# Optimization experiments

Measured on AMD Instinct MI355X. Metric: run time of the kernel, lower is better.

Reference implementation:

```python
import jax, jax.numpy as jnp
import numpy as np

DIM = 1024
HEADS = 16
DIM_HEAD = DIM // HEADS

def setup_inputs() -> dict:
    key = jax.random.key(0)
    k1, k2, k3 = jax.random.split(key, 3)
    x = jax.random.normal(k1, (2, 2048, DIM), dtype=jnp.float32)
    # nn.Linear(dim, 3*dim, bias=False): weight [3*dim, dim]; y = x @ W.T
    W_qkv = jax.random.normal(k2, (3 * DIM, DIM), dtype=jnp.float32) * (1.0 / np.sqrt(DIM))
    W_out = jax.random.normal(k3, (DIM, DIM), dtype=jnp.float32) * (1.0 / np.sqrt(DIM))
    return {"x": x, "W_qkv": W_qkv, "W_out": W_out}

def reference(x, W_qkv, W_out):
    b, s, _ = x.shape
    scale = DIM_HEAD ** -0.5
    qkv = x @ W_qkv.T                              # [b, s, 3*dim]
    q, k, v = jnp.split(qkv, 3, axis=-1)
    def to_heads(t):
        return t.reshape(b, s, HEADS, DIM_HEAD).transpose(0, 2, 1, 3)  # [b,h,s,d]
    q, k, v = map(to_heads, (q, k, v))
    scores = jnp.einsum('bhid,bhjd->bhij', q, k) * scale
    causal_mask = jnp.triu(jnp.ones((s, s), dtype=bool), k=1)
    scores = jnp.where(causal_mask, -jnp.inf, scores)
    attn = jax.nn.softmax(scores, axis=-1)
    out = jnp.einsum('bhij,bhjd->bhid', attn, v)
    out = out.transpose(0, 2, 1, 3).reshape(b, s, HEADS * DIM_HEAD)
    return out @ W_out.T
```

## Files before the change

kernel.cpp:

```cpp
#include <hip/hip_runtime.h>
#include <hip/hip_bf16.h>
#include <math.h>

using bf16 = __hip_bfloat16;
typedef __attribute__((ext_vector_type(8))) short bf16x8;
typedef __attribute__((ext_vector_type(4))) short bf16x4;
typedef __attribute__((ext_vector_type(4))) float f32x4;
typedef __attribute__((ext_vector_type(2))) int i32x2;

static __device__ __forceinline__ void gl_lds16(const void* g, void* l) {
  __builtin_amdgcn_global_load_lds(
      (const __attribute__((address_space(1))) unsigned int*)g,
      (__attribute__((address_space(3))) unsigned int*)l, 16, 0, 0);
}

#define MFMA16 __builtin_amdgcn_mfma_f32_16x16x32_bf16
#define MFMA16K16 __builtin_amdgcn_mfma_f32_16x16x16bf16_1k

static __device__ __forceinline__ short f2bf(float f) {
  return (short)((__builtin_bit_cast(unsigned int, f) + 0x8000u) >> 16);
}

__global__ __launch_bounds__(256) void cvt_all(
    const float* __restrict__ x, const float* __restrict__ wqkv,
    const float* __restrict__ wout, bf16* __restrict__ xb,
    bf16* __restrict__ wqkvb, bf16* __restrict__ woutb) {
  const int blk = blockIdx.x;
  const float* src;
  bf16* dst;
  int base;
  if (blk < 4096) {
    src = x; dst = xb; base = blk;
  } else if (blk < 7168) {
    src = wqkv; dst = wqkvb; base = blk - 4096;
  } else {
    src = wout; dst = woutb; base = blk - 7168;
  }
  const int i = (base * 256 + threadIdx.x) * 4;
  const float4 v = *(const float4*)(src + i);
  bf16x4 o;
  o.x = f2bf(v.x);
  o.y = f2bf(v.y);
  o.z = f2bf(v.z);
  o.w = f2bf(v.w);
  *(bf16x4*)(dst + i) = o;
}

template <int K>
static __device__ __forceinline__ void gemm_bt_acc(
    const bf16* __restrict__ A, const bf16* __restrict__ B,
    int rowA0, int rowB0, bf16* As, bf16* Bs, f32x4 acc[4][4]) {
  const int t = threadIdx.x;
  const int w = t >> 6, l = t & 63;
  const int quad = l >> 4, l16 = l & 15;
  const int wm = (w >> 1) * 64, wn = (w & 1) * 64;
  const int c0 = t, c1 = t + 256;
  const bf16* a0 = A + (size_t)(rowA0 + (c0 >> 2)) * K + (c0 & 3) * 8;
  const bf16* a1 = A + (size_t)(rowA0 + (c1 >> 2)) * K + (c1 & 3) * 8;
  const bf16* b0 = B + (size_t)(rowB0 + (c0 >> 2)) * K + (c0 & 3) * 8;
  const bf16* b1 = B + (size_t)(rowB0 + (c1 >> 2)) * K + (c1 & 3) * 8;
  for (int k0 = 0; k0 < K; k0 += 32) {
    __syncthreads();
    gl_lds16(a0 + k0, As + c0 * 8);
    gl_lds16(a1 + k0, As + c1 * 8);
    gl_lds16(b0 + k0, Bs + c0 * 8);
    gl_lds16(b1 + k0, Bs + c1 * 8);
    __syncthreads();
    bf16x8 af[4], bg[4];
#pragma unroll
    for (int i = 0; i < 4; i++)
      af[i] = *(const bf16x8*)(As + (wm + i * 16 + l16) * 32 + quad * 8);
#pragma unroll
    for (int j = 0; j < 4; j++)
      bg[j] = *(const bf16x8*)(Bs + (wn + j * 16 + l16) * 32 + quad * 8);
#pragma unroll
    for (int i = 0; i < 4; i++)
#pragma unroll
      for (int j = 0; j < 4; j++)
        acc[i][j] = MFMA16(af[i], bg[j], acc[i][j], 0, 0, 0);
  }
}

__global__ __launch_bounds__(256) void qkv_gemm(
    const bf16* __restrict__ x, const bf16* __restrict__ Wqkv,
    bf16* __restrict__ Qb, bf16* __restrict__ Kb, bf16* __restrict__ Vt) {
  __shared__ bf16 As[128 * 32];
  __shared__ bf16 Bs[128 * 32];
  f32x4 acc[4][4];
#pragma unroll
  for (int i = 0; i < 4; i++)
#pragma unroll
    for (int j = 0; j < 4; j++) acc[i][j] = (f32x4){0.f, 0.f, 0.f, 0.f};
  const int bm = blockIdx.x, bn = blockIdx.y;
  gemm_bt_acc<1024>(x, Wqkv, bm * 128, bn * 128, As, Bs, acc);

  const int t = threadIdx.x, w = t >> 6, l = t & 63;
  const int quad = l >> 4, l16 = l & 15;
  const int wm = (w >> 1) * 64, wn = (w & 1) * 64;
#pragma unroll
  for (int i = 0; i < 4; i++) {
    const int m0 = bm * 128 + wm + i * 16 + quad * 4;
    const int b = m0 >> 11, s0 = m0 & 2047;
#pragma unroll
    for (int j = 0; j < 4; j++) {
      const int n = bn * 128 + wn + j * 16 + l16;
      const int which = n >> 10;
      const int nn = n & 1023;
      const int h = nn >> 6, d = nn & 63;
      const int bh = b * 16 + h;
      if (which == 2) {
        bf16x4 v4;
#pragma unroll
        for (int r = 0; r < 4; r++)
          v4[r] = (short)__builtin_bit_cast(unsigned short,
                                            __float2bfloat16(acc[i][j][r]));
        *(bf16x4*)(Vt + ((size_t)bh * 64 + d) * 2048 + s0) = v4;
      } else {
        const float sc = (which == 0) ? 0.125f : 1.0f;
        bf16* dst = (which == 0) ? Qb : Kb;
#pragma unroll
        for (int r = 0; r < 4; r++)
          dst[((size_t)bh * 2048 + s0 + r) * 64 + d] =
              __float2bfloat16(acc[i][j][r] * sc);
      }
    }
  }
}

__global__ __launch_bounds__(256, 4) void attn_kernel(
    const bf16* __restrict__ Qb, const bf16* __restrict__ Kb,
    const bf16* __restrict__ Vt, bf16* __restrict__ attn) {
  __shared__ bf16 Ks[128 * 64];
  __shared__ bf16 Vts[64 * 128];
  const int x = blockIdx.x;
  const int bh = x & 31;
  const int T = x >> 5;
  const int s = T >> 3, r = T & 7;
  const int qt = s * 8 + ((s & 1) ? 7 - r : r);
  const int q0 = qt * 64;
  const int t = threadIdx.x, w = t >> 6, l = t & 63;
  const int quad = l >> 4, l16 = l & 15;
  const bf16x4 ones = {16256, 16256, 16256, 16256};
  const int b = bh >> 4, h = bh & 15;

  const int qrow = q0 + w * 16 + l16;
  const bf16* Qg = Qb + ((size_t)bh * 2048 + qrow) * 64 + quad * 8;
  bf16x8 qreg[2];
  qreg[0] = *(const bf16x8*)(Qg);
  qreg[1] = *(const bf16x8*)(Qg + 32);

  f32x4 oacc[4];
  f32x4 lacc = (f32x4){0.f, 0.f, 0.f, 0.f};
#pragma unroll
  for (int md = 0; md < 4; md++) oacc[md] = (f32x4){0.f, 0.f, 0.f, 0.f};

  const int njj = (qt + 2) >> 1;
  for (int jj = 0; jj < njj; jj++) {
    const int j0 = jj * 128;
    __syncthreads();
    const bf16* Kg = Kb + ((size_t)bh * 2048 + j0) * 64;
#pragma unroll
    for (int c = t; c < 1024; c += 256) {
      const int row = c >> 3, pos = c & 7;
      gl_lds16(Kg + (row * 8 + (pos ^ (row & 7))) * 8, Ks + c * 8);
    }
    const bf16* Vg = Vt + (size_t)bh * 64 * 2048 + j0;
#pragma unroll
    for (int c = t; c < 1024; c += 256) {
      const int d = c >> 4, pos = c & 15;
      gl_lds16(Vg + (size_t)d * 2048 + ((pos ^ (d & 15)) * 8), Vts + c * 8);
    }
    __syncthreads();

    f32x4 sacc[8];
#pragma unroll
    for (int mt = 0; mt < 8; mt++) sacc[mt] = (f32x4){0.f, 0.f, 0.f, 0.f};
#pragma unroll
    for (int kk = 0; kk < 2; kk++) {
#pragma unroll
      for (int mt = 0; mt < 8; mt++) {
        const int row = mt * 16 + l16;
        const int pos = (kk * 4 + quad) ^ (row & 7);
        bf16x8 kf = *(const bf16x8*)(Ks + row * 64 + pos * 8);
        sacc[mt] = MFMA16(kf, qreg[kk], sacc[mt], 0, 0, 0);
      }
    }

    bf16x4 pfrag[8];
    if (jj == njj - 1) {
      const int qi = q0 + w * 16 + l16;
#pragma unroll
      for (int mt = 0; mt < 8; mt++) {
        unsigned rb[4];
#pragma unroll
        for (int r2 = 0; r2 < 4; r2++) {
          const int sg = j0 + mt * 16 + quad * 4 + r2;
          const float p = (sg <= qi) ? __expf(sacc[mt][r2]) : 0.f;
          rb[r2] = __builtin_bit_cast(unsigned, p) + 0x8000u;
        }
        i32x2 pk;
        pk.x = (int)__builtin_amdgcn_perm(rb[1], rb[0], 0x07060302u);
        pk.y = (int)__builtin_amdgcn_perm(rb[3], rb[2], 0x07060302u);
        pfrag[mt] = __builtin_bit_cast(bf16x4, pk);
      }
    } else {
#pragma unroll
      for (int mt = 0; mt < 8; mt++) {
        unsigned rb[4];
#pragma unroll
        for (int r2 = 0; r2 < 4; r2++) {
          const float p = __expf(sacc[mt][r2]);
          rb[r2] = __builtin_bit_cast(unsigned, p) + 0x8000u;
        }
        i32x2 pk;
        pk.x = (int)__builtin_amdgcn_perm(rb[1], rb[0], 0x07060302u);
        pk.y = (int)__builtin_amdgcn_perm(rb[3], rb[2], 0x07060302u);
        pfrag[mt] = __builtin_bit_cast(bf16x4, pk);
      }
    }

#pragma unroll
    for (int kt = 0; kt < 8; kt++) {
      lacc = MFMA16K16(ones, pfrag[kt], lacc, 0, 0, 0);
#pragma unroll
      for (int md = 0; md < 4; md++) {
        const int d = md * 16 + l16;
        const int pos = (kt * 2 + (quad >> 1)) ^ (d & 15);
        bf16x4 va = *(const bf16x4*)(Vts + d * 128 + pos * 8 + (quad & 1) * 4);
        oacc[md] = MFMA16K16(va, pfrag[kt], oacc[md], 0, 0, 0);
      }
    }
  }

  const float inv = 1.0f / lacc[0];
#pragma unroll
  for (int md = 0; md < 4; md++) {
    bf16x4 o4;
#pragma unroll
    for (int r2 = 0; r2 < 4; r2++) o4[r2] = f2bf(oacc[md][r2] * inv);
    *(bf16x4*)(attn + ((size_t)b * 2048 + qrow) * 1024 + h * 64 + md * 16 +
               quad * 4) = o4;
  }
}

__global__ __launch_bounds__(256) void out_gemm(
    const bf16* __restrict__ attn, const bf16* __restrict__ Wout,
    float* __restrict__ out) {
  __shared__ bf16 As[128 * 32];
  __shared__ bf16 Bs[64 * 32];
  f32x4 acc[4][2];
#pragma unroll
  for (int i = 0; i < 4; i++)
#pragma unroll
    for (int j = 0; j < 2; j++) acc[i][j] = (f32x4){0.f, 0.f, 0.f, 0.f};
  const int bm = blockIdx.x, bn = blockIdx.y;
  const int t = threadIdx.x, w = t >> 6, l = t & 63;
  const int quad = l >> 4, l16 = l & 15;
  const int wm = (w >> 1) * 64, wn = (w & 1) * 32;
  const int c0 = t, c1 = t + 256;
  const bf16* a0 = attn + (size_t)(bm * 128 + (c0 >> 2)) * 1024 + (c0 & 3) * 8;
  const bf16* a1 = attn + (size_t)(bm * 128 + (c1 >> 2)) * 1024 + (c1 & 3) * 8;
  const bf16* b0 = Wout + (size_t)(bn * 64 + (t >> 2)) * 1024 + (t & 3) * 8;
  for (int k0 = 0; k0 < 1024; k0 += 32) {
    __syncthreads();
    gl_lds16(a0 + k0, As + c0 * 8);
    gl_lds16(a1 + k0, As + c1 * 8);
    gl_lds16(b0 + k0, Bs + t * 8);
    __syncthreads();
    bf16x8 af[4], bg[2];
#pragma unroll
    for (int i = 0; i < 4; i++)
      af[i] = *(const bf16x8*)(As + (wm + i * 16 + l16) * 32 + quad * 8);
#pragma unroll
    for (int j = 0; j < 2; j++)
      bg[j] = *(const bf16x8*)(Bs + (wn + j * 16 + l16) * 32 + quad * 8);
#pragma unroll
    for (int i = 0; i < 4; i++)
#pragma unroll
      for (int j = 0; j < 2; j++)
        acc[i][j] = MFMA16(af[i], bg[j], acc[i][j], 0, 0, 0);
  }
#pragma unroll
  for (int i = 0; i < 4; i++) {
#pragma unroll
    for (int j = 0; j < 2; j++) {
      const int n = bn * 64 + wn + j * 16 + l16;
#pragma unroll
      for (int r = 0; r < 4; r++) {
        const int m = bm * 128 + wm + i * 16 + quad * 4 + r;
        out[(size_t)m * 1024 + n] = acc[i][j][r];
      }
    }
  }
}

extern "C" void kernel_launch(void* const* d_in, const int* in_sizes, int n_in,
                              void* d_out, int out_size, void* d_ws, size_t ws_size,
                              hipStream_t stream) {
  const float* x = (const float*)d_in[0];
  const float* Wqkv = (const float*)d_in[1];
  const float* Wout = (const float*)d_in[2];
  float* out = (float*)d_out;

  char* ws = (char*)d_ws;
  const size_t MB = 1024 * 1024;
  bf16* xb = (bf16*)(ws + 0 * MB);
  bf16* at = (bf16*)(ws + 0 * MB);
  bf16* Wqkvb = (bf16*)(ws + 8 * MB);
  bf16* Woutb = (bf16*)(ws + 14 * MB);
  bf16* Qb = (bf16*)(ws + 16 * MB);
  bf16* Kb = (bf16*)(ws + 24 * MB);
  bf16* Vt = (bf16*)(ws + 32 * MB);

  cvt_all<<<8192, 256, 0, stream>>>(x, Wqkv, Wout, xb, Wqkvb, Woutb);
  qkv_gemm<<<dim3(32, 24), 256, 0, stream>>>(xb, Wqkvb, Qb, Kb, Vt);
  attn_kernel<<<1024, 256, 0, stream>>>(Qb, Kb, Vt, at);
  out_gemm<<<dim3(32, 16), 256, 0, stream>>>(at, Woutb, out);
}
```

Baseline: 164.1 us.

## Halve attention query tile and split key tiles across wave pairs

Each attention block now covers 32 query rows instead of 64, which doubles the grid to 2048 blocks. Within a block, two wave pairs each handle half of every 128-key tile. The partial output and row-sum accumulators are then combined through shared memory before normalisation, and launch bounds are raised to allow five blocks per CU. The aim is better load balance and occupancy for the causal workload, at the cost of loading each K/V tile for fewer queries and an extra LDS reduction at the end.

```diff
diff --git a/kernel.cpp b/kernel.cpp
--- a/kernel.cpp
+++ b/kernel.cpp
@@ -127,7 +127,7 @@
   }
 }
 
-__global__ __launch_bounds__(256, 4) void attn_kernel(
+__global__ __launch_bounds__(256, 5) void attn_kernel(
     const bf16* __restrict__ Qb, const bf16* __restrict__ Kb,
     const bf16* __restrict__ Vt, bf16* __restrict__ attn) {
   __shared__ bf16 Ks[128 * 64];
@@ -137,13 +137,15 @@
   const int T = x >> 5;
   const int s = T >> 3, r = T & 7;
   const int qt = s * 8 + ((s & 1) ? 7 - r : r);
-  const int q0 = qt * 64;
+  const int q0 = qt * 32;
   const int t = threadIdx.x, w = t >> 6, l = t & 63;
   const int quad = l >> 4, l16 = l & 15;
+  const int qh = w & 1;
+  const int kh = w >> 1;
   const bf16x4 ones = {16256, 16256, 16256, 16256};
   const int b = bh >> 4, h = bh & 15;
 
-  const int qrow = q0 + w * 16 + l16;
+  const int qrow = q0 + qh * 16 + l16;
   const bf16* Qg = Qb + ((size_t)bh * 2048 + qrow) * 64 + quad * 8;
   bf16x8 qreg[2];
   qreg[0] = *(const bf16x8*)(Qg);
@@ -154,7 +156,7 @@
 #pragma unroll
   for (int md = 0; md < 4; md++) oacc[md] = (f32x4){0.f, 0.f, 0.f, 0.f};
 
-  const int njj = (qt + 2) >> 1;
+  const int njj = (qt + 4) >> 2;
   for (int jj = 0; jj < njj; jj++) {
     const int j0 = jj * 128;
     __syncthreads();
@@ -172,74 +174,92 @@
     }
     __syncthreads();
 
-    f32x4 sacc[8];
-#pragma unroll
-    for (int mt = 0; mt < 8; mt++) sacc[mt] = (f32x4){0.f, 0.f, 0.f, 0.f};
+    f32x4 sacc[4];
+#pragma unroll
+    for (int m = 0; m < 4; m++) sacc[m] = (f32x4){0.f, 0.f, 0.f, 0.f};
 #pragma unroll
     for (int kk = 0; kk < 2; kk++) {
 #pragma unroll
-      for (int mt = 0; mt < 8; mt++) {
-        const int row = mt * 16 + l16;
-        const int pos = (kk * 4 + quad) ^ (row & 7);
+      for (int m = 0; m < 4; m++) {
+        const int row = (kh * 4 + m) * 16 + l16;
+        const int pos = (kk * 4 + quad) ^ (l16 & 7);
         bf16x8 kf = *(const bf16x8*)(Ks + row * 64 + pos * 8);
-        sacc[mt] = MFMA16(kf, qreg[kk], sacc[mt], 0, 0, 0);
-      }
-    }
-
-    bf16x4 pfrag[8];
+        sacc[m] = MFMA16(kf, qreg[kk], sacc[m], 0, 0, 0);
+      }
+    }
+
+    bf16x4 pfrag[4];
     if (jj == njj - 1) {
-      const int qi = q0 + w * 16 + l16;
-#pragma unroll
-      for (int mt = 0; mt < 8; mt++) {
+#pragma unroll
+      for (int m = 0; m < 4; m++) {
         unsigned rb[4];
 #pragma unroll
         for (int r2 = 0; r2 < 4; r2++) {
-          const int sg = j0 + mt * 16 + quad * 4 + r2;
-          const float p = (sg <= qi) ? __expf(sacc[mt][r2]) : 0.f;
+          const int sg = j0 + (kh * 4 + m) * 16 + quad * 4 + r2;
+          const float p = (sg <= qrow) ? __expf(sacc[m][r2]) : 0.f;
           rb[r2] = __builtin_bit_cast(unsigned, p) + 0x8000u;
         }
         i32x2 pk;
         pk.x = (int)__builtin_amdgcn_perm(rb[1], rb[0], 0x07060302u);
         pk.y = (int)__builtin_amdgcn_perm(rb[3], rb[2], 0x07060302u);
-        pfrag[mt] = __builtin_bit_cast(bf16x4, pk);
+        pfrag[m] = __builtin_bit_cast(bf16x4, pk);
       }
     } else {
 #pragma unroll
-      for (int mt = 0; mt < 8; mt++) {
+      for (int m = 0; m < 4; m++) {
         unsigned rb[4];
 #pragma unroll
         for (int r2 = 0; r2 < 4; r2++) {
-          const float p = __expf(sacc[mt][r2]);
+          const float p = __expf(sacc[m][r2]);
           rb[r2] = __builtin_bit_cast(unsigned, p) + 0x8000u;
         }
         i32x2 pk;
         pk.x = (int)__builtin_amdgcn_perm(rb[1], rb[0], 0x07060302u);
         pk.y = (int)__builtin_amdgcn_perm(rb[3], rb[2], 0x07060302u);
-        pfrag[mt] = __builtin_bit_cast(bf16x4, pk);
-      }
-    }
-
-#pragma unroll
-    for (int kt = 0; kt < 8; kt++) {
-      lacc = MFMA16K16(ones, pfrag[kt], lacc, 0, 0, 0);
+        pfrag[m] = __builtin_bit_cast(bf16x4, pk);
+      }
+    }
+
+#pragma unroll
+    for (int c = 0; c < 4; c++) {
+      const int kt = kh * 4 + c;
+      lacc = MFMA16K16(ones, pfrag[c], lacc, 0, 0, 0);
 #pragma unroll
       for (int md = 0; md < 4; md++) {
         const int d = md * 16 + l16;
-        const int pos = (kt * 2 + (quad >> 1)) ^ (d & 15);
+        const int pos = (kt * 2 + (quad >> 1)) ^ l16;
         bf16x4 va = *(const bf16x4*)(Vts + d * 128 + pos * 8 + (quad & 1) * 4);
-        oacc[md] = MFMA16K16(va, pfrag[kt], oacc[md], 0, 0, 0);
-      }
-    }
-  }
-
-  const float inv = 1.0f / lacc[0];
-#pragma unroll
-  for (int md = 0; md < 4; md++) {
-    bf16x4 o4;
-#pragma unroll
-    for (int r2 = 0; r2 < 4; r2++) o4[r2] = f2bf(oacc[md][r2] * inv);
-    *(bf16x4*)(attn + ((size_t)b * 2048 + qrow) * 1024 + h * 64 + md * 16 +
-               quad * 4) = o4;
+        oacc[md] = MFMA16K16(va, pfrag[c], oacc[md], 0, 0, 0);
+      }
+    }
+  }
+
+  __syncthreads();
+  float* red = (float*)Ks;
+  if (kh == 1) {
+    const int base = (qh * 64 + l) * 20;
+#pragma unroll
+    for (int md = 0; md < 4; md++) *(f32x4*)(red + base + md * 4) = oacc[md];
+    red[base + 16] = lacc[0];
+  }
+  __syncthreads();
+  if (kh == 0) {
+    const int base = (qh * 64 + l) * 20;
+#pragma unroll
+    for (int md = 0; md < 4; md++) {
+      const f32x4 o2 = *(const f32x4*)(red + base + md * 4);
+#pragma unroll
+      for (int r2 = 0; r2 < 4; r2++) oacc[md][r2] += o2[r2];
+    }
+    const float inv = 1.0f / (lacc[0] + red[base + 16]);
+#pragma unroll
+    for (int md = 0; md < 4; md++) {
+      bf16x4 o4;
+#pragma unroll
+      for (int r2 = 0; r2 < 4; r2++) o4[r2] = f2bf(oacc[md][r2] * inv);
+      *(bf16x4*)(attn + ((size_t)b * 2048 + qrow) * 1024 + h * 64 + md * 16 +
+                 quad * 4) = o4;
+    }
   }
 }
 
@@ -314,6 +334,6 @@
 
   cvt_all<<<8192, 256, 0, stream>>>(x, Wqkv, Wout, xb, Wqkvb, Woutb);
   qkv_gemm<<<dim3(32, 24), 256, 0, stream>>>(xb, Wqkvb, Qb, Kb, Vt);
-  attn_kernel<<<1024, 256, 0, stream>>>(Qb, Kb, Vt, at);
+  attn_kernel<<<2048, 256, 0, stream>>>(Qb, Kb, Vt, at);
   out_gemm<<<dim3(32, 16), 256, 0, stream>>>(at, Woutb, out);
 }
```

After: 173.6 us. 5.8% more time.

## Split attention key range across warps with LDS reduction instead of shared K/V tiles

Applied to the files above, without the earlier changes.

The attention kernel no longer stages K and V tiles in LDS. Each warp now handles all 64 query rows for its own 32-key slice of every 128-key block. It loads K and V fragments straight from global memory into registers, and the warps' partial outputs and row sums are combined through an LDS reduction at the end. This removes the per-iteration barriers and LDS staging. In exchange it costs more registers (occupancy hint lowered to 3), uncoalesced direct global loads, and a final cross-warp reduction serialized on one warp.

```diff
diff --git a/kernel.cpp b/kernel.cpp
--- a/kernel.cpp
+++ b/kernel.cpp
@@ -127,11 +127,10 @@
   }
 }
 
-__global__ __launch_bounds__(256, 4) void attn_kernel(
+__global__ __launch_bounds__(256, 3) void attn_kernel(
     const bf16* __restrict__ Qb, const bf16* __restrict__ Kb,
     const bf16* __restrict__ Vt, bf16* __restrict__ attn) {
-  __shared__ bf16 Ks[128 * 64];
-  __shared__ bf16 Vts[64 * 128];
+  __shared__ float red[3 * 64 * 68];
   const int x = blockIdx.x;
   const int bh = x & 31;
   const int T = x >> 5;
@@ -143,103 +142,147 @@
   const bf16x4 ones = {16256, 16256, 16256, 16256};
   const int b = bh >> 4, h = bh & 15;
 
-  const int qrow = q0 + w * 16 + l16;
-  const bf16* Qg = Qb + ((size_t)bh * 2048 + qrow) * 64 + quad * 8;
-  bf16x8 qreg[2];
-  qreg[0] = *(const bf16x8*)(Qg);
-  qreg[1] = *(const bf16x8*)(Qg + 32);
-
-  f32x4 oacc[4];
-  f32x4 lacc = (f32x4){0.f, 0.f, 0.f, 0.f};
-#pragma unroll
-  for (int md = 0; md < 4; md++) oacc[md] = (f32x4){0.f, 0.f, 0.f, 0.f};
+  bf16x8 qreg[4][2];
+#pragma unroll
+  for (int qf = 0; qf < 4; qf++) {
+    const bf16* Qg = Qb + ((size_t)bh * 2048 + q0 + qf * 16 + l16) * 64 + quad * 8;
+    qreg[qf][0] = *(const bf16x8*)(Qg);
+    qreg[qf][1] = *(const bf16x8*)(Qg + 32);
+  }
+
+  f32x4 oacc[4][4];
+  f32x4 lacc[4];
+#pragma unroll
+  for (int qf = 0; qf < 4; qf++) {
+    lacc[qf] = (f32x4){0.f, 0.f, 0.f, 0.f};
+#pragma unroll
+    for (int md = 0; md < 4; md++) oacc[md][qf] = (f32x4){0.f, 0.f, 0.f, 0.f};
+  }
 
   const int njj = (qt + 2) >> 1;
   for (int jj = 0; jj < njj; jj++) {
     const int j0 = jj * 128;
-    __syncthreads();
-    const bf16* Kg = Kb + ((size_t)bh * 2048 + j0) * 64;
-#pragma unroll
-    for (int c = t; c < 1024; c += 256) {
-      const int row = c >> 3, pos = c & 7;
-      gl_lds16(Kg + (row * 8 + (pos ^ (row & 7))) * 8, Ks + c * 8);
-    }
-    const bf16* Vg = Vt + (size_t)bh * 64 * 2048 + j0;
-#pragma unroll
-    for (int c = t; c < 1024; c += 256) {
-      const int d = c >> 4, pos = c & 15;
-      gl_lds16(Vg + (size_t)d * 2048 + ((pos ^ (d & 15)) * 8), Vts + c * 8);
-    }
-    __syncthreads();
-
-    f32x4 sacc[8];
-#pragma unroll
-    for (int mt = 0; mt < 8; mt++) sacc[mt] = (f32x4){0.f, 0.f, 0.f, 0.f};
-#pragma unroll
-    for (int kk = 0; kk < 2; kk++) {
-#pragma unroll
-      for (int mt = 0; mt < 8; mt++) {
-        const int row = mt * 16 + l16;
-        const int pos = (kk * 4 + quad) ^ (row & 7);
-        bf16x8 kf = *(const bf16x8*)(Ks + row * 64 + pos * 8);
-        sacc[mt] = MFMA16(kf, qreg[kk], sacc[mt], 0, 0, 0);
-      }
-    }
-
-    bf16x4 pfrag[8];
+    bf16x8 kf[2][2];
+#pragma unroll
+    for (int mt = 0; mt < 2; mt++) {
+      const bf16* Kg =
+          Kb + ((size_t)bh * 2048 + j0 + w * 32 + mt * 16 + l16) * 64 + quad * 8;
+      kf[mt][0] = *(const bf16x8*)(Kg);
+      kf[mt][1] = *(const bf16x8*)(Kg + 32);
+    }
+
+    f32x4 sacc[2][4];
+#pragma unroll
+    for (int mt = 0; mt < 2; mt++)
+#pragma unroll
+      for (int qf = 0; qf < 4; qf++) sacc[mt][qf] = (f32x4){0.f, 0.f, 0.f, 0.f};
+#pragma unroll
+    for (int kk = 0; kk < 2; kk++)
+#pragma unroll
+      for (int mt = 0; mt < 2; mt++)
+#pragma unroll
+        for (int qf = 0; qf < 4; qf++)
+          sacc[mt][qf] = MFMA16(kf[mt][kk], qreg[qf][kk], sacc[mt][qf], 0, 0, 0);
+
+    bf16x4 va[4][2];
+#pragma unroll
+    for (int md = 0; md < 4; md++) {
+      const bf16* Vg =
+          Vt + ((size_t)bh * 64 + md * 16 + l16) * 2048 + j0 + w * 32 + quad * 4;
+      va[md][0] = *(const bf16x4*)(Vg);
+      va[md][1] = *(const bf16x4*)(Vg + 16);
+    }
+
+    bf16x4 pfrag[2][4];
     if (jj == njj - 1) {
-      const int qi = q0 + w * 16 + l16;
-#pragma unroll
-      for (int mt = 0; mt < 8; mt++) {
-        unsigned rb[4];
-#pragma unroll
-        for (int r2 = 0; r2 < 4; r2++) {
-          const int sg = j0 + mt * 16 + quad * 4 + r2;
-          const float p = (sg <= qi) ? __expf(sacc[mt][r2]) : 0.f;
-          rb[r2] = __builtin_bit_cast(unsigned, p) + 0x8000u;
+#pragma unroll
+      for (int mt = 0; mt < 2; mt++)
+#pragma unroll
+        for (int qf = 0; qf < 4; qf++) {
+          const int qi = q0 + qf * 16 + l16;
+          unsigned rb[4];
+#pragma unroll
+          for (int r2 = 0; r2 < 4; r2++) {
+            const int sg = j0 + w * 32 + mt * 16 + quad * 4 + r2;
+            const float p = (sg <= qi) ? __expf(sacc[mt][qf][r2]) : 0.f;
+            rb[r2] = __builtin_bit_cast(unsigned, p) + 0x8000u;
+          }
+          i32x2 pk;
+          pk.x = (int)__builtin_amdgcn_perm(rb[1], rb[0], 0x07060302u);
+          pk.y = (int)__builtin_amdgcn_perm(rb[3], rb[2], 0x07060302u);
+          pfrag[mt][qf] = __builtin_bit_cast(bf16x4, pk);
         }
-        i32x2 pk;
-        pk.x = (int)__builtin_amdgcn_perm(rb[1], rb[0], 0x07060302u);
-        pk.y = (int)__builtin_amdgcn_perm(rb[3], rb[2], 0x07060302u);
-        pfrag[mt] = __builtin_bit_cast(bf16x4, pk);
-      }
     } else {
 #pragma unroll
-      for (int mt = 0; mt < 8; mt++) {
-        unsigned rb[4];
-#pragma unroll
-        for (int r2 = 0; r2 < 4; r2++) {
-          const float p = __expf(sacc[mt][r2]);
-          rb[r2] = __builtin_bit_cast(unsigned, p) + 0x8000u;
+      for (int mt = 0; mt < 2; mt++)
+#pragma unroll
+        for (int qf = 0; qf < 4; qf++) {
+          unsigned rb[4];
+#pragma unroll
+          for (int r2 = 0; r2 < 4; r2++) {
+            const float p = __expf(sacc[mt][qf][r2]);
+            rb[r2] = __builtin_bit_cast(unsigned, p) + 0x8000u;
+          }
+          i32x2 pk;
+          pk.x = (int)__builtin_amdgcn_perm(rb[1], rb[0], 0x07060302u);
+          pk.y = (int)__builtin_amdgcn_perm(rb[3], rb[2], 0x07060302u);
+          pfrag[mt][qf] = __builtin_bit_cast(bf16x4, pk);
         }
-        i32x2 pk;
-        pk.x = (int)__builtin_amdgcn_perm(rb[1], rb[0], 0x07060302u);
-        pk.y = (int)__builtin_amdgcn_perm(rb[3], rb[2], 0x07060302u);
-        pfrag[mt] = __builtin_bit_cast(bf16x4, pk);
-      }
-    }
-
-#pragma unroll
-    for (int kt = 0; kt < 8; kt++) {
-      lacc = MFMA16K16(ones, pfrag[kt], lacc, 0, 0, 0);
+    }
+
+#pragma unroll
+    for (int mt = 0; mt < 2; mt++)
+#pragma unroll
+      for (int qf = 0; qf < 4; qf++) {
+        lacc[qf] = MFMA16K16(ones, pfrag[mt][qf], lacc[qf], 0, 0, 0);
+#pragma unroll
+        for (int md = 0; md < 4; md++)
+          oacc[md][qf] =
+              MFMA16K16(va[md][mt], pfrag[mt][qf], oacc[md][qf], 0, 0, 0);
+      }
+  }
+
+  if (w > 0) {
+    float* rg = red + (w - 1) * 4352;
+#pragma unroll
+    for (int qf = 0; qf < 4; qf++) {
+#pragma unroll
+      for (int md = 0; md < 4; md++)
+        *(f32x4*)(rg + (qf * 16 + l16) * 68 + md * 16 + quad * 4) =
+            oacc[md][qf];
+      if (quad == 0) rg[(qf * 16 + l16) * 68 + 64] = lacc[qf][0];
+    }
+  }
+  __syncthreads();
+  if (w == 0) {
+#pragma unroll
+    for (int reg = 0; reg < 3; reg++) {
+      const float* rg = red + reg * 4352;
+#pragma unroll
+      for (int qf = 0; qf < 4; qf++) {
+#pragma unroll
+        for (int md = 0; md < 4; md++) {
+          const f32x4 o2 =
+              *(const f32x4*)(rg + (qf * 16 + l16) * 68 + md * 16 + quad * 4);
+#pragma unroll
+          for (int r2 = 0; r2 < 4; r2++) oacc[md][qf][r2] += o2[r2];
+        }
+        lacc[qf][0] += rg[(qf * 16 + l16) * 68 + 64];
+      }
+    }
+#pragma unroll
+    for (int qf = 0; qf < 4; qf++) {
+      const float inv = 1.0f / lacc[qf][0];
+      const int qrow = q0 + qf * 16 + l16;
 #pragma unroll
       for (int md = 0; md < 4; md++) {
-        const int d = md * 16 + l16;
-        const int pos = (kt * 2 + (quad >> 1)) ^ (d & 15);
-        bf16x4 va = *(const bf16x4*)(Vts + d * 128 + pos * 8 + (quad & 1) * 4);
-        oacc[md] = MFMA16K16(va, pfrag[kt], oacc[md], 0, 0, 0);
-      }
-    }
-  }
-
-  const float inv = 1.0f / lacc[0];
-#pragma unroll
-  for (int md = 0; md < 4; md++) {
-    bf16x4 o4;
-#pragma unroll
-    for (int r2 = 0; r2 < 4; r2++) o4[r2] = f2bf(oacc[md][r2] * inv);
-    *(bf16x4*)(attn + ((size_t)b * 2048 + qrow) * 1024 + h * 64 + md * 16 +
-               quad * 4) = o4;
+        bf16x4 o4;
+#pragma unroll
+        for (int r2 = 0; r2 < 4; r2++) o4[r2] = f2bf(oacc[md][qf][r2] * inv);
+        *(bf16x4*)(attn + ((size_t)b * 2048 + qrow) * 1024 + h * 64 + md * 16 +
+                   quad * 4) = o4;
+      }
+    }
   }
 }
 
```

Result: slower. 192.3 us (+17.2%).

## Double-buffer K/V tiles in attention and schedule heaviest query tiles first

Applied to the files above, without the earlier changes.

The attention kernel now keeps two LDS buffers for K and V^T tiles. It issues the async global-to-LDS loads for the next key block before computing on the current one, with a single barrier at the end of each iteration, so load latency can overlap with MFMA work. Block-to-query-tile mapping changes from a snake ordering to descending tile index, so the longest causal rows start first. Swizzle index expressions are simplified to equivalent forms. LDS use per block doubles, which may cut the number of resident blocks per CU below the launch-bounds target.

```diff
diff --git a/kernel.cpp b/kernel.cpp
--- a/kernel.cpp
+++ b/kernel.cpp
@@ -130,13 +130,11 @@
 __global__ __launch_bounds__(256, 4) void attn_kernel(
     const bf16* __restrict__ Qb, const bf16* __restrict__ Kb,
     const bf16* __restrict__ Vt, bf16* __restrict__ attn) {
-  __shared__ bf16 Ks[128 * 64];
-  __shared__ bf16 Vts[64 * 128];
+  __shared__ bf16 Ks[2][128 * 64];
+  __shared__ bf16 Vts[2][64 * 128];
   const int x = blockIdx.x;
   const int bh = x & 31;
-  const int T = x >> 5;
-  const int s = T >> 3, r = T & 7;
-  const int qt = s * 8 + ((s & 1) ? 7 - r : r);
+  const int qt = 31 - (x >> 5);
   const int q0 = qt * 64;
   const int t = threadIdx.x, w = t >> 6, l = t & 63;
   const int quad = l >> 4, l16 = l & 15;
@@ -149,28 +147,39 @@
   qreg[0] = *(const bf16x8*)(Qg);
   qreg[1] = *(const bf16x8*)(Qg + 32);
 
+  auto STAGE = [&](int jj, int buf) {
+    const int j0 = jj * 128;
+    const bf16* Kg = Kb + ((size_t)bh * 2048 + j0) * 64;
+    bf16* Ksb = &Ks[buf][0];
+#pragma unroll
+    for (int c = t; c < 1024; c += 256) {
+      const int row = c >> 3, pos = c & 7;
+      gl_lds16(Kg + (row * 8 + (pos ^ (row & 7))) * 8, Ksb + c * 8);
+    }
+    const bf16* Vg = Vt + (size_t)bh * 64 * 2048 + j0;
+    bf16* Vb = &Vts[buf][0];
+#pragma unroll
+    for (int c = t; c < 1024; c += 256) {
+      const int d = c >> 4, pos = c & 15;
+      gl_lds16(Vg + (size_t)d * 2048 + ((pos ^ (d & 15)) * 8), Vb + c * 8);
+    }
+  };
+
   f32x4 oacc[4];
   f32x4 lacc = (f32x4){0.f, 0.f, 0.f, 0.f};
 #pragma unroll
   for (int md = 0; md < 4; md++) oacc[md] = (f32x4){0.f, 0.f, 0.f, 0.f};
 
   const int njj = (qt + 2) >> 1;
+  STAGE(0, 0);
+  __syncthreads();
+
   for (int jj = 0; jj < njj; jj++) {
     const int j0 = jj * 128;
-    __syncthreads();
-    const bf16* Kg = Kb + ((size_t)bh * 2048 + j0) * 64;
-#pragma unroll
-    for (int c = t; c < 1024; c += 256) {
-      const int row = c >> 3, pos = c & 7;
-      gl_lds16(Kg + (row * 8 + (pos ^ (row & 7))) * 8, Ks + c * 8);
-    }
-    const bf16* Vg = Vt + (size_t)bh * 64 * 2048 + j0;
-#pragma unroll
-    for (int c = t; c < 1024; c += 256) {
-      const int d = c >> 4, pos = c & 15;
-      gl_lds16(Vg + (size_t)d * 2048 + ((pos ^ (d & 15)) * 8), Vts + c * 8);
-    }
-    __syncthreads();
+    const int cur = jj & 1;
+    if (jj + 1 < njj) STAGE(jj + 1, cur ^ 1);
+    const bf16* Ksb = &Ks[cur][0];
+    const bf16* Vb = &Vts[cur][0];
 
     f32x4 sacc[8];
 #pragma unroll
@@ -180,22 +189,21 @@
 #pragma unroll
       for (int mt = 0; mt < 8; mt++) {
         const int row = mt * 16 + l16;
-        const int pos = (kk * 4 + quad) ^ (row & 7);
-        bf16x8 kf = *(const bf16x8*)(Ks + row * 64 + pos * 8);
+        const int pos = (kk * 4 + quad) ^ (l16 & 7);
+        bf16x8 kf = *(const bf16x8*)(Ksb + row * 64 + pos * 8);
         sacc[mt] = MFMA16(kf, qreg[kk], sacc[mt], 0, 0, 0);
       }
     }
 
     bf16x4 pfrag[8];
     if (jj == njj - 1) {
-      const int qi = q0 + w * 16 + l16;
 #pragma unroll
       for (int mt = 0; mt < 8; mt++) {
         unsigned rb[4];
 #pragma unroll
         for (int r2 = 0; r2 < 4; r2++) {
           const int sg = j0 + mt * 16 + quad * 4 + r2;
-          const float p = (sg <= qi) ? __expf(sacc[mt][r2]) : 0.f;
+          const float p = (sg <= qrow) ? __expf(sacc[mt][r2]) : 0.f;
           rb[r2] = __builtin_bit_cast(unsigned, p) + 0x8000u;
         }
         i32x2 pk;
@@ -225,11 +233,13 @@
 #pragma unroll
       for (int md = 0; md < 4; md++) {
         const int d = md * 16 + l16;
-        const int pos = (kt * 2 + (quad >> 1)) ^ (d & 15);
-        bf16x4 va = *(const bf16x4*)(Vts + d * 128 + pos * 8 + (quad & 1) * 4);
+        const int pos = (kt * 2 + (quad >> 1)) ^ l16;
+        bf16x4 va = *(const bf16x4*)(Vb + d * 128 + pos * 8 + (quad & 1) * 4);
         oacc[md] = MFMA16K16(va, pfrag[kt], oacc[md], 0, 0, 0);
       }
     }
+
+    __syncthreads();
   }
 
   const float inv = 1.0f / lacc[0];
```

Result: slower. 169.1 us (+3.0%).
